# Kernel tuning notes

Hardware: AMD Instinct MI355X
Metric: run time of the kernel (lower is better)

## Reference

```python
import jax, jax.numpy as jnp
import numpy as np

B, T, C, O = 32, 2048, 1152, 29  # batch, temporal len, in channels (sum(data_length)), classes


def setup_inputs() -> dict:
    key = jax.random.key(0)
    k1, k2, k3, k4 = jax.random.split(key, 4)
    x = jax.random.normal(k1, (B, T, C), dtype=jnp.float32)
    # per-sample valid length, >=1 to avoid div-by-zero
    length = jax.random.randint(k2, (B,), 1, T + 1, dtype=jnp.int64)
    # Conv1d(C, O, 1) weight [O, C, 1] -> stored as [O, C]; bias [O]
    W = jax.random.normal(k3, (O, C), dtype=jnp.float32) * (1.0 / np.sqrt(C))
    b = jax.random.normal(k4, (O,), dtype=jnp.float32) * 0.01
    return {"x": x, "length": length, "W": W, "b": b}


def reference(x, length, W, b):
    # x: [B, T, C]; scale/shift then 1x1 conv (pointwise linear) then sum over T.
    # Linearity lets us fuse: sum_t (W @ (x/64 - 2) + b) == einsum + T*b.
    y = x / 64.0 - 2.0                      # [B, T, C]
    z = jnp.einsum('btc,oc->bo', y, W)      # temporal-summed projection [B, O]
    z = z + jnp.asarray(x.shape[1], z.dtype) * b
    return z / length.astype(z.dtype)[:, None]
```

## Files before the change

kernel.cpp:

```cpp
#include <hip/hip_runtime.h>
#include <hip/hip_bf16.h>


#define PB 32
#define PT 2048
#define PC 1152
#define PO 29
#define TSPLIT 32
#define C4 (PC / 4)

__global__ __launch_bounds__(256) void sum_t_kernel(const float* __restrict__ x,
                                                    float* __restrict__ s) {
    const int b   = blockIdx.x;
    const int p   = blockIdx.y;
    const int tid = threadIdx.x;

    const float4* x4 = (const float4*)(x + (size_t)b * PT * PC);

    float4 acc0 = make_float4(0.f, 0.f, 0.f, 0.f);
    float4 acc1 = make_float4(0.f, 0.f, 0.f, 0.f);

    const int tBeg = p * (PT / TSPLIT);
    const int tEnd = tBeg + (PT / TSPLIT);

#pragma unroll 4
    for (int t = tBeg; t < tEnd; ++t) {
        const float4* row = x4 + (size_t)t * C4;
        float4 v = row[tid];
        acc0.x += v.x; acc0.y += v.y; acc0.z += v.z; acc0.w += v.w;
        if (tid < C4 - 256) {
            float4 v2 = row[256 + tid];
            acc1.x += v2.x; acc1.y += v2.y; acc1.z += v2.z; acc1.w += v2.w;
        }
    }

    float* sb = s + b * PC;
    atomicAdd(&sb[tid * 4 + 0], acc0.x);
    atomicAdd(&sb[tid * 4 + 1], acc0.y);
    atomicAdd(&sb[tid * 4 + 2], acc0.z);
    atomicAdd(&sb[tid * 4 + 3], acc0.w);
    if (tid < C4 - 256) {
        atomicAdd(&sb[(256 + tid) * 4 + 0], acc1.x);
        atomicAdd(&sb[(256 + tid) * 4 + 1], acc1.y);
        atomicAdd(&sb[(256 + tid) * 4 + 2], acc1.z);
        atomicAdd(&sb[(256 + tid) * 4 + 3], acc1.w);
    }
}

__global__ __launch_bounds__(64) void proj_kernel(const float* __restrict__ s,
                                                  const float* __restrict__ W,
                                                  const float* __restrict__ bias,
                                                  const int* __restrict__ length,
                                                  float* __restrict__ out) {
    const int o    = blockIdx.x;
    const int b    = blockIdx.y;
    const int lane = threadIdx.x;

    const float* Wo = W + o * PC;
    const float* sb = s + b * PC;

    float dot = 0.f, wsum = 0.f;
#pragma unroll
    for (int c = lane; c < PC; c += 64) {
        float w = Wo[c];
        dot  += w * sb[c];
        wsum += w;
    }

#pragma unroll
    for (int off = 32; off > 0; off >>= 1) {
        dot  += __shfl_down(dot,  off);
        wsum += __shfl_down(wsum, off);
    }

    if (lane == 0) {
        float z = dot * (1.0f / 64.0f)
                - 2.0f * (float)PT * wsum
                + (float)PT * bias[o];
        out[b * PO + o] = z / (float)length[b];
    }
}

extern "C" void kernel_launch(void* const* d_in, const int* in_sizes, int n_in,
                              void* d_out, int out_size, void* d_ws, size_t ws_size,
                              hipStream_t stream) {
    const float* x      = (const float*)d_in[0];
    const int*   length = (const int*)d_in[1];
    const float* W      = (const float*)d_in[2];
    const float* bias   = (const float*)d_in[3];
    float*       out    = (float*)d_out;
    float*       s      = (float*)d_ws;

    hipMemsetAsync(s, 0, (size_t)PB * PC * sizeof(float), stream);

    dim3 g1(PB, TSPLIT);
    sum_t_kernel<<<g1, 256, 0, stream>>>(x, s);

    dim3 g2(PO, PB);
    proj_kernel<<<g2, 64, 0, stream>>>(s, W, bias, length, out);
}
```

Before: 437.4 us.

## Replace atomic accumulation with per-slab partials and a fused finish kernel

The temporal-sum kernel now uses 288 threads, so each thread owns one float4 column with no divergent second load. It writes per-slab partial sums to the workspace instead of atomically adding into a zeroed buffer, which removes the memset and the atomics. A single per-batch finish kernel reduces the 32 partials, applies the scale and shift into shared memory, and computes all 29 projections. The cost is an extra read of the partial buffer (about 4.7 MB). The main x read is still memory-bound, so gains are likely limited to launch and atomic overhead.

```diff
diff --git a/kernel.cpp b/kernel.cpp
--- a/kernel.cpp
+++ b/kernel.cpp
@@ -1,5 +1,4 @@
 #include <hip/hip_runtime.h>
-#include <hip/hip_bf16.h>
 
 
 #define PB 32
@@ -7,77 +6,76 @@
 #define PC 1152
 #define PO 29
 #define TSPLIT 32
+#define ROWS (PT / TSPLIT)
 #define C4 (PC / 4)
 
-__global__ __launch_bounds__(256) void sum_t_kernel(const float* __restrict__ x,
-                                                    float* __restrict__ s) {
+__global__ __launch_bounds__(288) void sum_slab_kernel(const float* __restrict__ x,
+                                                       float* __restrict__ sp) {
     const int b   = blockIdx.x;
     const int p   = blockIdx.y;
     const int tid = threadIdx.x;
 
-    const float4* x4 = (const float4*)(x + (size_t)b * PT * PC);
+    const float4* __restrict__ src =
+        (const float4*)x + ((size_t)b * PT + (size_t)p * ROWS) * C4 + tid;
 
-    float4 acc0 = make_float4(0.f, 0.f, 0.f, 0.f);
-    float4 acc1 = make_float4(0.f, 0.f, 0.f, 0.f);
+    float4 acc = make_float4(0.f, 0.f, 0.f, 0.f);
 
-    const int tBeg = p * (PT / TSPLIT);
-    const int tEnd = tBeg + (PT / TSPLIT);
-
-#pragma unroll 4
-    for (int t = tBeg; t < tEnd; ++t) {
-        const float4* row = x4 + (size_t)t * C4;
-        float4 v = row[tid];
-        acc0.x += v.x; acc0.y += v.y; acc0.z += v.z; acc0.w += v.w;
-        if (tid < C4 - 256) {
-            float4 v2 = row[256 + tid];
-            acc1.x += v2.x; acc1.y += v2.y; acc1.z += v2.z; acc1.w += v2.w;
-        }
+#pragma unroll 8
+    for (int t = 0; t < ROWS; ++t) {
+        float4 v = src[(size_t)t * C4];
+        acc.x += v.x; acc.y += v.y; acc.z += v.z; acc.w += v.w;
     }
 
-    float* sb = s + b * PC;
-    atomicAdd(&sb[tid * 4 + 0], acc0.x);
-    atomicAdd(&sb[tid * 4 + 1], acc0.y);
-    atomicAdd(&sb[tid * 4 + 2], acc0.z);
-    atomicAdd(&sb[tid * 4 + 3], acc0.w);
-    if (tid < C4 - 256) {
-        atomicAdd(&sb[(256 + tid) * 4 + 0], acc1.x);
-        atomicAdd(&sb[(256 + tid) * 4 + 1], acc1.y);
-        atomicAdd(&sb[(256 + tid) * 4 + 2], acc1.z);
-        atomicAdd(&sb[(256 + tid) * 4 + 3], acc1.w);
-    }
+    float4* __restrict__ dst = (float4*)sp + ((size_t)b * TSPLIT + p) * C4 + tid;
+    *dst = acc;
 }
 
-__global__ __launch_bounds__(64) void proj_kernel(const float* __restrict__ s,
-                                                  const float* __restrict__ W,
-                                                  const float* __restrict__ bias,
-                                                  const int* __restrict__ length,
-                                                  float* __restrict__ out) {
-    const int o    = blockIdx.x;
-    const int b    = blockIdx.y;
-    const int lane = threadIdx.x;
+__global__ __launch_bounds__(256) void finish_kernel(const float* __restrict__ sp,
+                                                     const float* __restrict__ W,
+                                                     const float* __restrict__ bias,
+                                                     const int* __restrict__ length,
+                                                     float* __restrict__ out) {
+    const int b   = blockIdx.x;
+    const int tid = threadIdx.x;
 
-    const float* Wo = W + o * PC;
-    const float* sb = s + b * PC;
+    __shared__ float s_hat[PC];
 
-    float dot = 0.f, wsum = 0.f;
+    const float4* __restrict__ spb = (const float4*)sp + (size_t)b * TSPLIT * C4;
+
+    for (int c4 = tid; c4 < C4; c4 += 256) {
+        float4 a = make_float4(0.f, 0.f, 0.f, 0.f);
+#pragma unroll 8
+        for (int p = 0; p < TSPLIT; ++p) {
+            float4 v = spb[(size_t)p * C4 + c4];
+            a.x += v.x; a.y += v.y; a.z += v.z; a.w += v.w;
+        }
+        const float scale = 1.0f / 64.0f;
+        const float shift = -2.0f * (float)PT;
+        s_hat[c4 * 4 + 0] = a.x * scale + shift;
+        s_hat[c4 * 4 + 1] = a.y * scale + shift;
+        s_hat[c4 * 4 + 2] = a.z * scale + shift;
+        s_hat[c4 * 4 + 3] = a.w * scale + shift;
+    }
+    __syncthreads();
+
+    const int wave = tid >> 6;
+    const int lane = tid & 63;
+    const float inv_len = 1.0f / (float)length[b];
+
+    for (int o = wave; o < PO; o += 4) {
+        const float* __restrict__ Wo = W + (size_t)o * PC;
+        float dot = 0.f;
 #pragma unroll
-    for (int c = lane; c < PC; c += 64) {
-        float w = Wo[c];
-        dot  += w * sb[c];
-        wsum += w;
-    }
-
+        for (int c = lane; c < PC; c += 64) {
+            dot += Wo[c] * s_hat[c];
+        }
 #pragma unroll
-    for (int off = 32; off > 0; off >>= 1) {
-        dot  += __shfl_down(dot,  off);
-        wsum += __shfl_down(wsum, off);
-    }
-
-    if (lane == 0) {
-        float z = dot * (1.0f / 64.0f)
-                - 2.0f * (float)PT * wsum
-                + (float)PT * bias[o];
-        out[b * PO + o] = z / (float)length[b];
+        for (int off = 32; off > 0; off >>= 1) {
+            dot += __shfl_down(dot, off);
+        }
+        if (lane == 0) {
+            out[b * PO + o] = (dot + (float)PT * bias[o]) * inv_len;
+        }
     }
 }
 
@@ -89,13 +87,10 @@
     const float* W      = (const float*)d_in[2];
     const float* bias   = (const float*)d_in[3];
     float*       out    = (float*)d_out;
-    float*       s      = (float*)d_ws;
-
-    hipMemsetAsync(s, 0, (size_t)PB * PC * sizeof(float), stream);
+    float*       sp     = (float*)d_ws;
 
     dim3 g1(PB, TSPLIT);
-    sum_t_kernel<<<g1, 256, 0, stream>>>(x, s);
+    sum_slab_kernel<<<g1, C4, 0, stream>>>(x, sp);
 
-    dim3 g2(PO, PB);
-    proj_kernel<<<g2, 64, 0, stream>>>(s, W, bias, length, out);
+    finish_kernel<<<PB, 256, 0, stream>>>(sp, W, bias, length, out);
 }
```

Result: slower. 457.5 us (+4.6%).
